# Kernel optimization log

Measured on AMD Instinct MI355X. Metric: run time of the kernel, lower is better.

The kernel has to match this reference:

```python
import jax, jax.numpy as jnp
import numpy as np

N_NODES = 100000
N_EDGES = 1600000
F_IN = 128
HID = 128
N_CLS = 40


def setup_inputs() -> dict:
    key = jax.random.key(0)
    ks = jax.random.split(key, 11)
    s = 0.05
    return {
        "X": jax.random.normal(ks[0], (N_NODES, F_IN), dtype=jnp.float32),
        "edge_index": jax.random.randint(ks[1], (2, N_EDGES), 0, N_NODES, dtype=jnp.int64),
        "enc_W": jax.random.normal(ks[2], (HID, F_IN), dtype=jnp.float32) * s,
        "enc_b": jax.random.normal(ks[3], (HID,), dtype=jnp.float32) * s,
        "W1": jax.random.normal(ks[4], (HID, HID), dtype=jnp.float32) * s,
        "b1": jax.random.normal(ks[5], (HID,), dtype=jnp.float32) * s,
        "W2": jax.random.normal(ks[6], (HID, HID), dtype=jnp.float32) * s,
        "b2": jax.random.normal(ks[7], (HID,), dtype=jnp.float32) * s,
        "dec_W": jax.random.normal(ks[8], (N_CLS, HID), dtype=jnp.float32) * s,
        "dec_b": jax.random.normal(ks[9], (N_CLS,), dtype=jnp.float32) * s,
    }


def reference(X, edge_index, enc_W, enc_b, W1, b1, W2, b2, dec_W, dec_b):
    N = X.shape[0]
    # --- add self-loops (PyG GCNConv default) ---
    loop = jnp.arange(N, dtype=edge_index.dtype)
    src = jnp.concatenate([edge_index[0], loop])  # message sources
    dst = jnp.concatenate([edge_index[1], loop])  # aggregation targets
    # --- symmetric normalization: D^{-1/2} A_hat D^{-1/2} ---
    deg = jax.ops.segment_sum(jnp.ones_like(src, dtype=X.dtype), dst, num_segments=N)
    dinv = jnp.where(deg > 0, jax.lax.rsqrt(deg), 0.0)
    norm = dinv[src] * dinv[dst]  # [E+N]

    def gcn_conv(x, W, b):
        h = x @ W.T                               # [N,H] linear transform
        msg = h[src] * norm[:, None]              # gather + scale  [E+N,H]
        agg = jax.ops.segment_sum(msg, dst, num_segments=N)  # scatter-sum
        return agg + b

    x = X @ enc_W.T + enc_b                       # encoder (single Linear)
    x = jax.nn.relu(gcn_conv(x, W1, b1))
    x = jax.nn.relu(gcn_conv(x, W2, b2))
    logits = x @ dec_W.T + dec_b                  # decoder (single Linear)
    return jax.nn.log_softmax(logits, axis=1)
```

## Files before the change

### kernel.cpp

```cpp
#include <hip/hip_runtime.h>
#include <hip/hip_bf16.h>
#include <cstdint>

typedef __bf16 bf16x8 __attribute__((ext_vector_type(8)));
typedef float  f32x4  __attribute__((ext_vector_type(4)));


__global__ __launch_bounds__(256) void bucket_hist_kernel(const int* __restrict__ dst,
                                                          int* __restrict__ bhist,
                                                          int E, int NBK, int shift) {
    __shared__ int lh[1024];
    int t = threadIdx.x;
    for (int i = t; i < 1024; i += 256) lh[i] = 0;
    __syncthreads();
#pragma unroll
    for (int v = 0; v < 4; ++v) {
        int idx = blockIdx.x * 4096 + (v * 256 + t) * 4;
        if (idx + 3 < E) {
            int4 d = *reinterpret_cast<const int4*>(&dst[idx]);
            atomicAdd(&lh[d.x >> shift], 1);
            atomicAdd(&lh[d.y >> shift], 1);
            atomicAdd(&lh[d.z >> shift], 1);
            atomicAdd(&lh[d.w >> shift], 1);
        } else {
            for (int k = 0; k < 4; ++k)
                if (idx + k < E) atomicAdd(&lh[dst[idx + k] >> shift], 1);
        }
    }
    __syncthreads();
    for (int i = t; i < NBK; i += 256)
        if (lh[i]) atomicAdd(&bhist[i], lh[i]);
}

__global__ __launch_bounds__(256) void bucket_scan_kernel(const int* __restrict__ bhist,
                                                          int* __restrict__ bbase,
                                                          int* __restrict__ bcur,
                                                          int NBK, int* __restrict__ offsetsN, int E) {
    int t = threadIdx.x;
    int v0[4]; int s = 0;
#pragma unroll
    for (int k = 0; k < 4; ++k) { int i = t * 4 + k; v0[k] = (i < NBK) ? bhist[i] : 0; s += v0[k]; }
    int lane = t & 63, w = t >> 6;
    int v = s;
#pragma unroll
    for (int o = 1; o < 64; o <<= 1) { int u = __shfl_up(v, o); if (lane >= o) v += u; }
    __shared__ int ws[4];
    if (lane == 63) ws[w] = v;
    __syncthreads();
    if (t == 0) { int r = 0; for (int i = 0; i < 4; ++i) { int x = ws[i]; ws[i] = r; r += x; } }
    __syncthreads();
    int run = ws[w] + (v - s);
#pragma unroll
    for (int k = 0; k < 4; ++k) {
        int i = t * 4 + k;
        if (i < NBK) { bbase[i] = run; bcur[i] = run; run += v0[k]; }
    }
    if (t == 255) bbase[NBK] = E;
    if (t == 0)   *offsetsN = E;
}

__global__ __launch_bounds__(256) void bin_edges_kernel(const int* __restrict__ src,
                                                        const int* __restrict__ dst,
                                                        int* __restrict__ bcur,
                                                        uint2* __restrict__ binned,
                                                        int E, int NBK, int shift) {
    __shared__ int lh[1024];
    int t = threadIdx.x;
    for (int i = t; i < 1024; i += 256) lh[i] = 0;
    __syncthreads();
    int sv[32], dv[32], rk[32];
#pragma unroll
    for (int v = 0; v < 8; ++v) {
        int idx = blockIdx.x * 8192 + (v * 256 + t) * 4;
        if (idx + 3 < E) {
            int4 s4 = *reinterpret_cast<const int4*>(&src[idx]);
            int4 d4 = *reinterpret_cast<const int4*>(&dst[idx]);
            sv[v * 4 + 0] = s4.x; sv[v * 4 + 1] = s4.y; sv[v * 4 + 2] = s4.z; sv[v * 4 + 3] = s4.w;
            dv[v * 4 + 0] = d4.x; dv[v * 4 + 1] = d4.y; dv[v * 4 + 2] = d4.z; dv[v * 4 + 3] = d4.w;
        } else {
            for (int k = 0; k < 4; ++k) {
                sv[v * 4 + k] = (idx + k < E) ? src[idx + k] : 0;
                dv[v * 4 + k] = (idx + k < E) ? dst[idx + k] : -1;
            }
        }
    }
#pragma unroll
    for (int k = 0; k < 32; ++k)
        if (dv[k] >= 0) rk[k] = atomicAdd(&lh[dv[k] >> shift], 1);
    __syncthreads();
    for (int i = t; i < NBK; i += 256) {
        int c = lh[i];
        lh[i] = c ? atomicAdd(&bcur[i], c) : 0;
    }
    __syncthreads();
#pragma unroll
    for (int k = 0; k < 32; ++k) {
        if (dv[k] >= 0) {
            int b = dv[k] >> shift;
            binned[lh[b] + rk[k]] = make_uint2((unsigned)sv[k], (unsigned)dv[k]);
        }
    }
}

__global__ __launch_bounds__(256) void bucket_build_kernel(const uint2* __restrict__ binned,
                                                           const int* __restrict__ bbase,
                                                           int* __restrict__ csr_src,
                                                           int* __restrict__ offsets,
                                                           float* __restrict__ dinv,
                                                           int N, int shift) {
    int b = blockIdx.x;
    int t = threadIdx.x;
    int node0 = b << shift;
    int npb = min(1 << shift, N - node0);
    int bb = bbase[b], be = bbase[b + 1];
    __shared__ int ncnt[256], npre[256], ncur[256];
    ncnt[t] = 0;
    __syncthreads();
    for (int e = bb + t; e < be; e += 256) {
        uint2 p = binned[e];
        atomicAdd(&ncnt[p.y - node0], 1);
    }
    __syncthreads();
    int deg = (t < npb) ? ncnt[t] : 0;
    int v = deg;
    int lane = t & 63, w = t >> 6;
#pragma unroll
    for (int o = 1; o < 64; o <<= 1) { int u = __shfl_up(v, o); if (lane >= o) v += u; }
    __shared__ int ws[4];
    if (lane == 63) ws[w] = v;
    __syncthreads();
    if (t == 0) { int r = 0; for (int i = 0; i < 4; ++i) { int x = ws[i]; ws[i] = r; r += x; } }
    __syncthreads();
    int pre = bb + ws[w] + v - deg;
    npre[t] = pre; ncur[t] = 0;
    __syncthreads();
    for (int e = bb + t; e < be; e += 256) {
        uint2 p = binned[e];
        int l = p.y - node0;
        int r = atomicAdd(&ncur[l], 1);
        csr_src[npre[l] + r] = (int)p.x;
    }
    if (t < npb) {
        int node = node0 + t;
        offsets[node] = pre;
        dinv[node] = rsqrtf((float)(deg + 1));
    }
}

__global__ __launch_bounds__(128) void prep_weights_kernel(const float* __restrict__ W1,
                                                           const float* __restrict__ encW,
                                                           const float* __restrict__ encb,
                                                           const float* __restrict__ W2,
                                                           const float* __restrict__ decW,
                                                           __hip_bfloat16* __restrict__ Wfb,
                                                           float* __restrict__ bff,
                                                           __hip_bfloat16* __restrict__ W2b,
                                                           __hip_bfloat16* __restrict__ decWb) {
    int i = blockIdx.x;
    int j = threadIdx.x;
    const float* w1r = W1 + (size_t)i * 128;
    float s0 = 0.f, s1 = 0.f, s2 = 0.f, s3 = 0.f;
    for (int k = 0; k < 128; k += 4) {
        s0 += w1r[k + 0] * encW[(size_t)(k + 0) * 128 + j];
        s1 += w1r[k + 1] * encW[(size_t)(k + 1) * 128 + j];
        s2 += w1r[k + 2] * encW[(size_t)(k + 2) * 128 + j];
        s3 += w1r[k + 3] * encW[(size_t)(k + 3) * 128 + j];
    }
    Wfb[(size_t)i * 128 + j] = __float2bfloat16((s0 + s1) + (s2 + s3));
    W2b[(size_t)i * 128 + j] = __float2bfloat16(W2[(size_t)i * 128 + j]);
    if (i < 48) decWb[(size_t)i * 128 + j] = __float2bfloat16(i < 40 ? decW[(size_t)i * 128 + j] : 0.f);
    float t = w1r[j] * encb[j];
#pragma unroll
    for (int o = 32; o; o >>= 1) t += __shfl_down(t, o);
    __shared__ float red[2];
    if ((j & 63) == 0) red[j >> 6] = t;
    __syncthreads();
    if (j == 0) bff[i] = red[0] + red[1];
}

__device__ inline bf16x8 cvt8(float4 lo, float4 hi) {
    union { unsigned short u[8]; bf16x8 v; } t;
    t.u[0] = __builtin_bit_cast(unsigned short, __float2bfloat16(lo.x));
    t.u[1] = __builtin_bit_cast(unsigned short, __float2bfloat16(lo.y));
    t.u[2] = __builtin_bit_cast(unsigned short, __float2bfloat16(lo.z));
    t.u[3] = __builtin_bit_cast(unsigned short, __float2bfloat16(lo.w));
    t.u[4] = __builtin_bit_cast(unsigned short, __float2bfloat16(hi.x));
    t.u[5] = __builtin_bit_cast(unsigned short, __float2bfloat16(hi.y));
    t.u[6] = __builtin_bit_cast(unsigned short, __float2bfloat16(hi.z));
    t.u[7] = __builtin_bit_cast(unsigned short, __float2bfloat16(hi.w));
    return t.v;
}

__global__ __launch_bounds__(256) void gemm_enc_kernel(const float* __restrict__ Ain,
                                                       const __hip_bfloat16* __restrict__ W,
                                                       const float* __restrict__ bias,
                                                       const float* __restrict__ dscale,
                                                       __hip_bfloat16* __restrict__ out, int M) {
    int lane = threadIdx.x & 63;
    int wave = threadIdx.x >> 6;
    int row0 = blockIdx.x * 128 + wave * 32;
    int kgrp = lane >> 4, cl = lane & 15;

    bf16x8 afrag[2][4];
#pragma unroll
    for (int rt = 0; rt < 2; ++rt) {
        int ar = row0 + rt * 16 + cl;
        if (ar >= M) ar = M - 1;
        const float* Ar = Ain + (size_t)ar * 128;
#pragma unroll
        for (int c = 0; c < 4; ++c) {
            const float4* q = reinterpret_cast<const float4*>(Ar + (4 * c + kgrp) * 8);
            afrag[rt][c] = cvt8(q[0], q[1]);
        }
    }

    f32x4 acc[2][8];
#pragma unroll
    for (int rt = 0; rt < 2; ++rt)
#pragma unroll
        for (int t = 0; t < 8; ++t) acc[rt][t] = {0.f, 0.f, 0.f, 0.f};

#pragma unroll
    for (int c = 0; c < 4; ++c) {
#pragma unroll
        for (int t = 0; t < 8; ++t) {
            bf16x8 bfrag = reinterpret_cast<const bf16x8*>(W + (size_t)(t * 16 + cl) * 128)[4 * c + kgrp];
            acc[0][t] = __builtin_amdgcn_mfma_f32_16x16x32_bf16(afrag[0][c], bfrag, acc[0][t], 0, 0, 0);
            acc[1][t] = __builtin_amdgcn_mfma_f32_16x16x32_bf16(afrag[1][c], bfrag, acc[1][t], 0, 0, 0);
        }
    }

#pragma unroll
    for (int rt = 0; rt < 2; ++rt) {
        int rbase = row0 + rt * 16 + kgrp * 4;
#pragma unroll
        for (int i = 0; i < 4; ++i) {
            int r = rbase + i;
            float sc = dscale[(r < M) ? r : (M - 1)];
#pragma unroll
            for (int t = 0; t < 8; ++t) {
                int col = t * 16 + cl;
                float v = (acc[rt][t][i] + bias[col]) * sc;
                unsigned int uv = __builtin_bit_cast(unsigned short, __float2bfloat16(v));
                unsigned int pv = (unsigned int)__shfl_xor((int)uv, 1);
                if (!(lane & 1) && r < M)
                    *reinterpret_cast<unsigned int*>(out + (size_t)r * 128 + col) = (uv & 0xffffu) | (pv << 16);
            }
        }
    }
}

template<int NPW>
__device__ __forceinline__ void agg_phase(const __hip_bfloat16* __restrict__ h,
                                          const int* __restrict__ csr_src,
                                          const int* __restrict__ offsets,
                                          const float* __restrict__ dinv,
                                          const float* __restrict__ bias,
                                          unsigned* lds, int tile0, int N) {
    int w = threadIdx.x >> 6, lane = threadIdx.x & 63;
    int bc = lane * 2;
    float2 bb = *reinterpret_cast<const float2*>(&bias[bc]);
    int base = tile0 + w * NPW;
    int oidx = base + (lane < NPW ? lane : NPW);
    if (oidx > N) oidx = N;
    int off = offsets[oidx];

    for (int i = 0; i < NPW; ++i) {
        int node = base + i;
        bool live = node < N;
        int nd = live ? node : N - 1;
        int j0 = __builtin_amdgcn_readfirstlane(__shfl(off, i));
        int j1 = __builtin_amdgcn_readfirstlane(__shfl(off, i + 1));

        float ax[8], ay[8];
        unsigned q0 = *reinterpret_cast<const unsigned*>(&h[(size_t)nd * 128 + bc]);
        ax[0] = __builtin_bit_cast(float, q0 << 16);
        ay[0] = __builtin_bit_cast(float, q0 & 0xffff0000u);
#pragma unroll
        for (int k = 1; k < 8; ++k) { ax[k] = 0.f; ay[k] = 0.f; }
        int j = j0;
        for (; j + 8 <= j1; j += 8) {
            int s[8];
#pragma unroll
            for (int k = 0; k < 8; ++k) s[k] = csr_src[j + k];
            unsigned q[8];
#pragma unroll
            for (int k = 0; k < 8; ++k)
                q[k] = *reinterpret_cast<const unsigned*>(&h[(size_t)s[k] * 128 + bc]);
#pragma unroll
            for (int k = 0; k < 8; ++k) {
                ax[k] += __builtin_bit_cast(float, q[k] << 16);
                ay[k] += __builtin_bit_cast(float, q[k] & 0xffff0000u);
            }
        }
        for (; j < j1; ++j) {
            int s0 = csr_src[j];
            unsigned q1 = *reinterpret_cast<const unsigned*>(&h[(size_t)s0 * 128 + bc]);
            ax[0] += __builtin_bit_cast(float, q1 << 16);
            ay[0] += __builtin_bit_cast(float, q1 & 0xffff0000u);
        }
        float sx = ((ax[0] + ax[1]) + (ax[2] + ax[3])) + ((ax[4] + ax[5]) + (ax[6] + ax[7]));
        float sy = ((ay[0] + ay[1]) + (ay[2] + ay[3])) + ((ay[4] + ay[5]) + (ay[6] + ay[7]));
        float dd = dinv[nd];
        float ox = fmaxf(dd * sx + bb.x, 0.f);
        float oy = fmaxf(dd * sy + bb.y, 0.f);
        unsigned ow = (unsigned)__builtin_bit_cast(unsigned short, __float2bfloat16(ox)) |
                      ((unsigned)__builtin_bit_cast(unsigned short, __float2bfloat16(oy)) << 16);
        if (!live) ow = 0u;
        int row = w * NPW + i;
        lds[row * 64 + (lane ^ ((row & 15) << 2))] = ow;
    }
}

__global__ __launch_bounds__(512) void agg_gemm_kernel(const __hip_bfloat16* __restrict__ h,
                                                       const int* __restrict__ csr_src,
                                                       const int* __restrict__ offsets,
                                                       const float* __restrict__ dinv,
                                                       const float* __restrict__ bias,
                                                       const __hip_bfloat16* __restrict__ W,
                                                       __hip_bfloat16* __restrict__ out, int N) {
    __shared__ unsigned lds[32 * 64];
    int tile0 = blockIdx.x * 32;
    agg_phase<4>(h, csr_src, offsets, dinv, bias, lds, tile0, N);
    __syncthreads();

    int lane = threadIdx.x & 63, w = threadIdx.x >> 6;
    int kgrp = lane >> 4, cl = lane & 15;
    int rt = w & 1, cq = w >> 1;
    bf16x8 afrag[4];
#pragma unroll
    for (int c = 0; c < 4; ++c) {
        int kk = 4 * c + kgrp;
        int row = rt * 16 + cl;
        afrag[c] = *reinterpret_cast<const bf16x8*>(&lds[row * 64 + ((kk * 4) ^ (cl << 2))]);
    }
    f32x4 acc[2];
#pragma unroll
    for (int t = 0; t < 2; ++t) acc[t] = {0.f, 0.f, 0.f, 0.f};
#pragma unroll
    for (int c = 0; c < 4; ++c)
#pragma unroll
        for (int t = 0; t < 2; ++t) {
            bf16x8 bfrag = reinterpret_cast<const bf16x8*>(W + (size_t)(cq * 32 + t * 16 + cl) * 128)[4 * c + kgrp];
            acc[t] = __builtin_amdgcn_mfma_f32_16x16x32_bf16(afrag[c], bfrag, acc[t], 0, 0, 0);
        }
#pragma unroll
    for (int i = 0; i < 4; ++i) {
        int r = tile0 + rt * 16 + kgrp * 4 + i;
        float sc = dinv[(r < N) ? r : (N - 1)];
#pragma unroll
        for (int t = 0; t < 2; ++t) {
            int col = cq * 32 + t * 16 + cl;
            float v = acc[t][i] * sc;
            unsigned uv = __builtin_bit_cast(unsigned short, __float2bfloat16(v));
            unsigned pv = (unsigned)__shfl_xor((int)uv, 1);
            if (!(lane & 1) && r < N)
                *reinterpret_cast<unsigned*>(out + (size_t)r * 128 + col) = (uv & 0xffffu) | (pv << 16);
        }
    }
}

__global__ __launch_bounds__(512) void agg_dec_kernel(const __hip_bfloat16* __restrict__ h,
                                                      const int* __restrict__ csr_src,
                                                      const int* __restrict__ offsets,
                                                      const float* __restrict__ dinv,
                                                      const float* __restrict__ bias,
                                                      const __hip_bfloat16* __restrict__ Wd,
                                                      const float* __restrict__ bd,
                                                      float* __restrict__ out, int N) {
    __shared__ unsigned lds[32 * 64];
    int tile0 = blockIdx.x * 32;
    agg_phase<4>(h, csr_src, offsets, dinv, bias, lds, tile0, N);
    __syncthreads();

    int lane = threadIdx.x & 63, w = threadIdx.x >> 6;
    if (w >= 2) return;
    int kgrp = lane >> 4, cl = lane & 15;
    bf16x8 afrag[4];
#pragma unroll
    for (int c = 0; c < 4; ++c) {
        int kk = 4 * c + kgrp;
        int row = w * 16 + cl;
        afrag[c] = *reinterpret_cast<const bf16x8*>(&lds[row * 64 + ((kk * 4) ^ (cl << 2))]);
    }
    f32x4 acc[3];
#pragma unroll
    for (int t = 0; t < 3; ++t) acc[t] = {0.f, 0.f, 0.f, 0.f};
#pragma unroll
    for (int c = 0; c < 4; ++c)
#pragma unroll
        for (int t = 0; t < 3; ++t) {
            bf16x8 bfrag = reinterpret_cast<const bf16x8*>(Wd + (size_t)(t * 16 + cl) * 128)[4 * c + kgrp];
            acc[t] = __builtin_amdgcn_mfma_f32_16x16x32_bf16(afrag[c], bfrag, acc[t], 0, 0, 0);
        }

    float v[3][4];
#pragma unroll
    for (int t = 0; t < 3; ++t) {
        int col = t * 16 + cl;
        float bv = (col < 40) ? bd[col] : 0.f;
#pragma unroll
        for (int i = 0; i < 4; ++i)
            v[t][i] = (col < 40) ? (acc[t][i] + bv) : -INFINITY;
    }
#pragma unroll
    for (int i = 0; i < 4; ++i) {
        float m = fmaxf(fmaxf(v[0][i], v[1][i]), v[2][i]);
#pragma unroll
        for (int o = 1; o < 16; o <<= 1) m = fmaxf(m, __shfl_xor(m, o));
        float s = 0.f;
#pragma unroll
        for (int t = 0; t < 3; ++t) s += (v[t][i] > -INFINITY) ? __expf(v[t][i] - m) : 0.f;
#pragma unroll
        for (int o = 1; o < 16; o <<= 1) s += __shfl_xor(s, o);
        float lse = __logf(s);
        int r = tile0 + w * 16 + kgrp * 4 + i;
        if (r < N) {
#pragma unroll
            for (int t = 0; t < 3; ++t) {
                int col = t * 16 + cl;
                if (col < 40) out[(size_t)r * 40 + col] = v[t][i] - m - lse;
            }
        }
    }
}

extern "C" void kernel_launch(void* const* d_in, const int* in_sizes, int n_in,
                              void* d_out, int out_size, void* d_ws, size_t ws_size,
                              hipStream_t stream) {
    const float* X    = (const float*)d_in[0];
    const int*   ei   = (const int*)d_in[1];
    const float* encW = (const float*)d_in[2];
    const float* encb = (const float*)d_in[3];
    const float* W1   = (const float*)d_in[4];
    const float* b1   = (const float*)d_in[5];
    const float* W2   = (const float*)d_in[6];
    const float* b2   = (const float*)d_in[7];
    const float* decW = (const float*)d_in[8];
    const float* decb = (const float*)d_in[9];

    const int N = in_sizes[0] / 128;
    const int E = in_sizes[1] / 2;
    const int* src = ei;
    const int* dst = ei + E;

    int shift = 7;
    while ((((N - 1) >> shift) + 1) > 1024) ++shift;
    const int NBK = ((N - 1) >> shift) + 1;

    uint8_t* p = (uint8_t*)d_ws;
    auto carve = [&](size_t bytes) -> void* {
        uint8_t* r = p;
        p += (bytes + 255) & ~(size_t)255;
        return (void*)r;
    };
    int*   offsets = (int*)carve((size_t)(N + 1) * 4);
    float* dinv    = (float*)carve((size_t)N * 4);
    int*   bhist   = (int*)carve(1025 * 4);
    int*   bbase   = (int*)carve(1025 * 4);
    int*   bcur    = (int*)carve(1024 * 4);
    int*   csr_src = (int*)carve((size_t)E * 4);
    __hip_bfloat16* Wfb   = (__hip_bfloat16*)carve(16384 * 2);
    __hip_bfloat16* W2b   = (__hip_bfloat16*)carve(16384 * 2);
    __hip_bfloat16* decWb = (__hip_bfloat16*)carve(48 * 128 * 2);
    float*          bff   = (float*)carve(128 * 4);
    __hip_bfloat16* xb    = (__hip_bfloat16*)carve((size_t)N * 128 * 2);
    __hip_bfloat16* hb    = (__hip_bfloat16*)carve((size_t)N * 128 * 2);
    uint2* binned = (uint2*)xb;

    prep_weights_kernel<<<128, 128, 0, stream>>>(W1, encW, encb, W2, decW, Wfb, bff, W2b, decWb);

    hipMemsetAsync(bhist, 0, (size_t)NBK * 4, stream);
    bucket_hist_kernel<<<(E + 4095) / 4096, 256, 0, stream>>>(dst, bhist, E, NBK, shift);
    bucket_scan_kernel<<<1, 256, 0, stream>>>(bhist, bbase, bcur, NBK, &offsets[N], E);
    bin_edges_kernel<<<(E + 8191) / 8192, 256, 0, stream>>>(src, dst, bcur, binned, E, NBK, shift);
    bucket_build_kernel<<<NBK, 256, 0, stream>>>(binned, bbase, csr_src, offsets, dinv, N, shift);

    int gblocks = (N + 127) / 128;
    int tblocks = (N + 31) / 32;
    gemm_enc_kernel<<<gblocks, 256, 0, stream>>>(X, Wfb, bff, dinv, hb, N);
    agg_gemm_kernel<<<tblocks, 512, 0, stream>>>(hb, csr_src, offsets, dinv, b1, W2b, xb, N);
    agg_dec_kernel<<<tblocks, 512, 0, stream>>>(xb, csr_src, offsets, dinv, b2, decWb, decb,
                                                (float*)d_out, N);
}
```

Baseline: 254.2 us.

## Sort nodes by degree for aggregation and pack binned edges into one word

Result: slower. 531.7 us (+109.2%).

```diff
diff --git a/kernel.cpp b/kernel.cpp
--- a/kernel.cpp
+++ b/kernel.cpp
@@ -62,10 +62,11 @@
 __global__ __launch_bounds__(256) void bin_edges_kernel(const int* __restrict__ src,
                                                         const int* __restrict__ dst,
                                                         int* __restrict__ bcur,
-                                                        uint2* __restrict__ binned,
+                                                        unsigned* __restrict__ binned,
                                                         int E, int NBK, int shift) {
     __shared__ int lh[1024];
     int t = threadIdx.x;
+    int mask = (1 << shift) - 1;
     for (int i = t; i < 1024; i += 256) lh[i] = 0;
     __syncthreads();
     int sv[32], dv[32], rk[32];
@@ -97,12 +98,12 @@
     for (int k = 0; k < 32; ++k) {
         if (dv[k] >= 0) {
             int b = dv[k] >> shift;
-            binned[lh[b] + rk[k]] = make_uint2((unsigned)sv[k], (unsigned)dv[k]);
-        }
-    }
-}
-
-__global__ __launch_bounds__(256) void bucket_build_kernel(const uint2* __restrict__ binned,
+            binned[lh[b] + rk[k]] = ((unsigned)sv[k] << shift) | (unsigned)(dv[k] & mask);
+        }
+    }
+}
+
+__global__ __launch_bounds__(256) void bucket_build_kernel(const unsigned* __restrict__ binned,
                                                            const int* __restrict__ bbase,
                                                            int* __restrict__ csr_src,
                                                            int* __restrict__ offsets,
@@ -113,12 +114,13 @@
     int node0 = b << shift;
     int npb = min(1 << shift, N - node0);
     int bb = bbase[b], be = bbase[b + 1];
+    int mask = (1 << shift) - 1;
     __shared__ int ncnt[256], npre[256], ncur[256];
     ncnt[t] = 0;
     __syncthreads();
     for (int e = bb + t; e < be; e += 256) {
-        uint2 p = binned[e];
-        atomicAdd(&ncnt[p.y - node0], 1);
+        unsigned p = binned[e];
+        atomicAdd(&ncnt[p & mask], 1);
     }
     __syncthreads();
     int deg = (t < npb) ? ncnt[t] : 0;
@@ -135,16 +137,64 @@
     npre[t] = pre; ncur[t] = 0;
     __syncthreads();
     for (int e = bb + t; e < be; e += 256) {
-        uint2 p = binned[e];
-        int l = p.y - node0;
+        unsigned p = binned[e];
+        int l = p & mask;
         int r = atomicAdd(&ncur[l], 1);
-        csr_src[npre[l] + r] = (int)p.x;
+        csr_src[npre[l] + r] = (int)(p >> shift);
     }
     if (t < npb) {
         int node = node0 + t;
         offsets[node] = pre;
         dinv[node] = rsqrtf((float)(deg + 1));
     }
+}
+
+__global__ __launch_bounds__(256) void deg_hist_kernel(const int* __restrict__ offsets,
+                                                       int* __restrict__ dh, int N) {
+    __shared__ int lh[512];
+    int t = threadIdx.x;
+    lh[t] = 0; lh[t + 256] = 0;
+    __syncthreads();
+    int i = blockIdx.x * 256 + t;
+    if (i < N) {
+        int deg = offsets[i + 1] - offsets[i];
+        atomicAdd(&lh[min(deg, 511)], 1);
+    }
+    __syncthreads();
+    if (lh[t]) atomicAdd(&dh[t], lh[t]);
+    if (lh[t + 256]) atomicAdd(&dh[t + 256], lh[t + 256]);
+}
+
+__global__ __launch_bounds__(256) void deg_scan_kernel(const int* __restrict__ dh,
+                                                       int* __restrict__ dcur) {
+    int t = threadIdx.x;
+    int v0 = dh[2 * t], v1 = dh[2 * t + 1];
+    int s = v0 + v1;
+    int lane = t & 63, w = t >> 6;
+    int v = s;
+#pragma unroll
+    for (int o = 1; o < 64; o <<= 1) { int u = __shfl_up(v, o); if (lane >= o) v += u; }
+    __shared__ int ws[4];
+    if (lane == 63) ws[w] = v;
+    __syncthreads();
+    if (t == 0) { int r = 0; for (int i = 0; i < 4; ++i) { int x = ws[i]; ws[i] = r; r += x; } }
+    __syncthreads();
+    int run = ws[w] + (v - s);
+    dcur[2 * t] = run;
+    dcur[2 * t + 1] = run + v0;
+}
+
+__global__ __launch_bounds__(256) void deg_scatter_kernel(const int* __restrict__ offsets,
+                                                          int* __restrict__ dcur,
+                                                          int* __restrict__ dorder,
+                                                          int2* __restrict__ off_deg, int N) {
+    int i = blockIdx.x * 256 + threadIdx.x;
+    if (i >= N) return;
+    int o0 = offsets[i];
+    int deg = offsets[i + 1] - o0;
+    int pos = atomicAdd(&dcur[min(deg, 511)], 1);
+    dorder[pos] = i;
+    off_deg[pos] = make_int2(o0, deg);
 }
 
 __global__ __launch_bounds__(128) void prep_weights_kernel(const float* __restrict__ W1,
@@ -253,27 +303,33 @@
 template<int NPW>
 __device__ __forceinline__ void agg_phase(const __hip_bfloat16* __restrict__ h,
                                           const int* __restrict__ csr_src,
-                                          const int* __restrict__ offsets,
+                                          const int* __restrict__ dorder,
+                                          const int2* __restrict__ off_deg,
                                           const float* __restrict__ dinv,
                                           const float* __restrict__ bias,
-                                          unsigned* lds, int tile0, int N) {
+                                          unsigned* lds, int* ndid, int tile0, int N) {
     int w = threadIdx.x >> 6, lane = threadIdx.x & 63;
     int bc = lane * 2;
     float2 bb = *reinterpret_cast<const float2*>(&bias[bc]);
     int base = tile0 + w * NPW;
-    int oidx = base + (lane < NPW ? lane : NPW);
-    if (oidx > N) oidx = N;
-    int off = offsets[oidx];
+
+    int2 od = make_int2(0, 0);
+    int nid = -1;
+    if (lane < NPW && base + lane < N) {
+        od  = off_deg[base + lane];
+        nid = dorder[base + lane];
+    }
 
     for (int i = 0; i < NPW; ++i) {
-        int node = base + i;
-        bool live = node < N;
-        int nd = live ? node : N - 1;
-        int j0 = __builtin_amdgcn_readfirstlane(__shfl(off, i));
-        int j1 = __builtin_amdgcn_readfirstlane(__shfl(off, i + 1));
+        int nd = __builtin_amdgcn_readfirstlane(__shfl(nid, i));
+        int j0 = __builtin_amdgcn_readfirstlane(__shfl(od.x, i));
+        int dg = __builtin_amdgcn_readfirstlane(__shfl(od.y, i));
+        bool live = nd >= 0;
+        int nds = live ? nd : 0;
+        int j1 = j0 + dg;
 
         float ax[8], ay[8];
-        unsigned q0 = *reinterpret_cast<const unsigned*>(&h[(size_t)nd * 128 + bc]);
+        unsigned q0 = *reinterpret_cast<const unsigned*>(&h[(size_t)nds * 128 + bc]);
         ax[0] = __builtin_bit_cast(float, q0 << 16);
         ay[0] = __builtin_bit_cast(float, q0 & 0xffff0000u);
 #pragma unroll
@@ -301,7 +357,7 @@
         }
         float sx = ((ax[0] + ax[1]) + (ax[2] + ax[3])) + ((ax[4] + ax[5]) + (ax[6] + ax[7]));
         float sy = ((ay[0] + ay[1]) + (ay[2] + ay[3])) + ((ay[4] + ay[5]) + (ay[6] + ay[7]));
-        float dd = dinv[nd];
+        float dd = dinv[nds];
         float ox = fmaxf(dd * sx + bb.x, 0.f);
         float oy = fmaxf(dd * sy + bb.y, 0.f);
         unsigned ow = (unsigned)__builtin_bit_cast(unsigned short, __float2bfloat16(ox)) |
@@ -309,19 +365,22 @@
         if (!live) ow = 0u;
         int row = w * NPW + i;
         lds[row * 64 + (lane ^ ((row & 15) << 2))] = ow;
+        if (lane == 0) ndid[row] = nd;
     }
 }
 
 __global__ __launch_bounds__(512) void agg_gemm_kernel(const __hip_bfloat16* __restrict__ h,
                                                        const int* __restrict__ csr_src,
-                                                       const int* __restrict__ offsets,
+                                                       const int* __restrict__ dorder,
+                                                       const int2* __restrict__ off_deg,
                                                        const float* __restrict__ dinv,
                                                        const float* __restrict__ bias,
                                                        const __hip_bfloat16* __restrict__ W,
                                                        __hip_bfloat16* __restrict__ out, int N) {
     __shared__ unsigned lds[32 * 64];
+    __shared__ int ndid[32];
     int tile0 = blockIdx.x * 32;
-    agg_phase<4>(h, csr_src, offsets, dinv, bias, lds, tile0, N);
+    agg_phase<4>(h, csr_src, dorder, off_deg, dinv, bias, lds, ndid, tile0, N);
     __syncthreads();
 
     int lane = threadIdx.x & 63, w = threadIdx.x >> 6;
@@ -346,31 +405,34 @@
         }
 #pragma unroll
     for (int i = 0; i < 4; ++i) {
-        int r = tile0 + rt * 16 + kgrp * 4 + i;
-        float sc = dinv[(r < N) ? r : (N - 1)];
+        int row = rt * 16 + kgrp * 4 + i;
+        int node = ndid[row];
+        float sc = dinv[(node >= 0) ? node : 0];
 #pragma unroll
         for (int t = 0; t < 2; ++t) {
             int col = cq * 32 + t * 16 + cl;
             float v = acc[t][i] * sc;
             unsigned uv = __builtin_bit_cast(unsigned short, __float2bfloat16(v));
             unsigned pv = (unsigned)__shfl_xor((int)uv, 1);
-            if (!(lane & 1) && r < N)
-                *reinterpret_cast<unsigned*>(out + (size_t)r * 128 + col) = (uv & 0xffffu) | (pv << 16);
+            if (!(lane & 1) && node >= 0)
+                *reinterpret_cast<unsigned*>(out + (size_t)node * 128 + col) = (uv & 0xffffu) | (pv << 16);
         }
     }
 }
 
 __global__ __launch_bounds__(512) void agg_dec_kernel(const __hip_bfloat16* __restrict__ h,
                                                       const int* __restrict__ csr_src,
-                                                      const int* __restrict__ offsets,
+                                                      const int* __restrict__ dorder,
+                                                      const int2* __restrict__ off_deg,
                                                       const float* __restrict__ dinv,
                                                       const float* __restrict__ bias,
                                                       const __hip_bfloat16* __restrict__ Wd,
                                                       const float* __restrict__ bd,
                                                       float* __restrict__ out, int N) {
     __shared__ unsigned lds[32 * 64];
+    __shared__ int ndid[32];
     int tile0 = blockIdx.x * 32;
-    agg_phase<4>(h, csr_src, offsets, dinv, bias, lds, tile0, N);
+    agg_phase<4>(h, csr_src, dorder, off_deg, dinv, bias, lds, ndid, tile0, N);
     __syncthreads();
 
     int lane = threadIdx.x & 63, w = threadIdx.x >> 6;
@@ -414,12 +476,13 @@
 #pragma unroll
         for (int o = 1; o < 16; o <<= 1) s += __shfl_xor(s, o);
         float lse = __logf(s);
-        int r = tile0 + w * 16 + kgrp * 4 + i;
-        if (r < N) {
+        int row = w * 16 + kgrp * 4 + i;
+        int node = ndid[row];
+        if (node >= 0) {
 #pragma unroll
             for (int t = 0; t < 3; ++t) {
                 int col = t * 16 + cl;
-                if (col < 40) out[(size_t)r * 40 + col] = v[t][i] - m - lse;
+                if (col < 40) out[(size_t)node * 40 + col] = v[t][i] - m - lse;
             }
         }
     }
@@ -459,6 +522,10 @@
     int*   bhist   = (int*)carve(1025 * 4);
     int*   bbase   = (int*)carve(1025 * 4);
     int*   bcur    = (int*)carve(1024 * 4);
+    int*   dh      = (int*)carve(512 * 4);
+    int*   dcur    = (int*)carve(512 * 4);
+    int*   dorder  = (int*)carve((size_t)N * 4);
+    int2*  off_deg = (int2*)carve((size_t)N * 8);
     int*   csr_src = (int*)carve((size_t)E * 4);
     __hip_bfloat16* Wfb   = (__hip_bfloat16*)carve(16384 * 2);
     __hip_bfloat16* W2b   = (__hip_bfloat16*)carve(16384 * 2);
@@ -466,7 +533,7 @@
     float*          bff   = (float*)carve(128 * 4);
     __hip_bfloat16* xb    = (__hip_bfloat16*)carve((size_t)N * 128 * 2);
     __hip_bfloat16* hb    = (__hip_bfloat16*)carve((size_t)N * 128 * 2);
-    uint2* binned = (uint2*)xb;
+    unsigned* binned = (unsigned*)xb;
 
     prep_weights_kernel<<<128, 128, 0, stream>>>(W1, encW, encb, W2, decW, Wfb, bff, W2b, decWb);
 
@@ -476,10 +543,15 @@
     bin_edges_kernel<<<(E + 8191) / 8192, 256, 0, stream>>>(src, dst, bcur, binned, E, NBK, shift);
     bucket_build_kernel<<<NBK, 256, 0, stream>>>(binned, bbase, csr_src, offsets, dinv, N, shift);
 
+    hipMemsetAsync(dh, 0, 512 * 4, stream);
+    deg_hist_kernel<<<(N + 255) / 256, 256, 0, stream>>>(offsets, dh, N);
+    deg_scan_kernel<<<1, 256, 0, stream>>>(dh, dcur);
+    deg_scatter_kernel<<<(N + 255) / 256, 256, 0, stream>>>(offsets, dcur, dorder, off_deg, N);
+
     int gblocks = (N + 127) / 128;
     int tblocks = (N + 31) / 32;
     gemm_enc_kernel<<<gblocks, 256, 0, stream>>>(X, Wfb, bff, dinv, hb, N);
-    agg_gemm_kernel<<<tblocks, 512, 0, stream>>>(hb, csr_src, offsets, dinv, b1, W2b, xb, N);
-    agg_dec_kernel<<<tblocks, 512, 0, stream>>>(xb, csr_src, offsets, dinv, b2, decWb, decb,
+    agg_gemm_kernel<<<tblocks, 512, 0, stream>>>(hb, csr_src, dorder, off_deg, dinv, b1, W2b, xb, N);
+    agg_dec_kernel<<<tblocks, 512, 0, stream>>>(xb, csr_src, dorder, off_deg, dinv, b2, decWb, decb,
                                                 (float*)d_out, N);
 }
```

## Pack binned edges to 32-bit and software-pipeline neighbor gathers across nodes

Applied to the files above, without the earlier changes.

After: 231.6 us. 8.9% less time.

```diff
diff --git a/kernel.cpp b/kernel.cpp
--- a/kernel.cpp
+++ b/kernel.cpp
@@ -62,10 +62,11 @@
 __global__ __launch_bounds__(256) void bin_edges_kernel(const int* __restrict__ src,
                                                         const int* __restrict__ dst,
                                                         int* __restrict__ bcur,
-                                                        uint2* __restrict__ binned,
+                                                        unsigned* __restrict__ binned,
                                                         int E, int NBK, int shift) {
     __shared__ int lh[1024];
     int t = threadIdx.x;
+    int mask = (1 << shift) - 1;
     for (int i = t; i < 1024; i += 256) lh[i] = 0;
     __syncthreads();
     int sv[32], dv[32], rk[32];
@@ -97,12 +98,12 @@
     for (int k = 0; k < 32; ++k) {
         if (dv[k] >= 0) {
             int b = dv[k] >> shift;
-            binned[lh[b] + rk[k]] = make_uint2((unsigned)sv[k], (unsigned)dv[k]);
-        }
-    }
-}
-
-__global__ __launch_bounds__(256) void bucket_build_kernel(const uint2* __restrict__ binned,
+            binned[lh[b] + rk[k]] = ((unsigned)sv[k] << shift) | (unsigned)(dv[k] & mask);
+        }
+    }
+}
+
+__global__ __launch_bounds__(256) void bucket_build_kernel(const unsigned* __restrict__ binned,
                                                            const int* __restrict__ bbase,
                                                            int* __restrict__ csr_src,
                                                            int* __restrict__ offsets,
@@ -113,12 +114,13 @@
     int node0 = b << shift;
     int npb = min(1 << shift, N - node0);
     int bb = bbase[b], be = bbase[b + 1];
+    int mask = (1 << shift) - 1;
     __shared__ int ncnt[256], npre[256], ncur[256];
     ncnt[t] = 0;
     __syncthreads();
     for (int e = bb + t; e < be; e += 256) {
-        uint2 p = binned[e];
-        atomicAdd(&ncnt[p.y - node0], 1);
+        unsigned p = binned[e];
+        atomicAdd(&ncnt[p & mask], 1);
     }
     __syncthreads();
     int deg = (t < npb) ? ncnt[t] : 0;
@@ -135,10 +137,10 @@
     npre[t] = pre; ncur[t] = 0;
     __syncthreads();
     for (int e = bb + t; e < be; e += 256) {
-        uint2 p = binned[e];
-        int l = p.y - node0;
+        unsigned p = binned[e];
+        int l = p & mask;
         int r = atomicAdd(&ncur[l], 1);
-        csr_src[npre[l] + r] = (int)p.x;
+        csr_src[npre[l] + r] = (int)(p >> shift);
     }
     if (t < npb) {
         int node = node0 + t;
@@ -252,7 +254,7 @@
 
 template<int NPW>
 __device__ __forceinline__ void agg_phase(const __hip_bfloat16* __restrict__ h,
-                                          const int* __restrict__ csr_src,
+                                          const int* __restrict__ csr,
                                           const int* __restrict__ offsets,
                                           const float* __restrict__ dinv,
                                           const float* __restrict__ bias,
@@ -265,43 +267,77 @@
     if (oidx > N) oidx = N;
     int off = offsets[oidx];
 
+    int j0a[NPW], dga[NPW], nda[NPW];
+    unsigned qs[NPW];
+#pragma unroll
     for (int i = 0; i < NPW; ++i) {
         int node = base + i;
+        nda[i] = __builtin_amdgcn_readfirstlane((node < N) ? node : (N - 1));
+        j0a[i] = __builtin_amdgcn_readfirstlane(__shfl(off, i));
+        int j1 = __builtin_amdgcn_readfirstlane(__shfl(off, i + 1));
+        dga[i] = j1 - j0a[i];
+        qs[i] = *reinterpret_cast<const unsigned*>(&h[(size_t)nda[i] * 128 + bc]);
+    }
+    int sc[NPW][8];
+#pragma unroll
+    for (int i = 0; i < NPW; ++i)
+#pragma unroll
+        for (int k = 0; k < 8; ++k)
+            sc[i][k] = csr[j0a[i] + k];
+    unsigned qn[8];
+#pragma unroll
+    for (int k = 0; k < 8; ++k)
+        qn[k] = *reinterpret_cast<const unsigned*>(&h[(size_t)sc[0][k] * 128 + bc]);
+
+#pragma unroll
+    for (int i = 0; i < NPW; ++i) {
+        int j0 = j0a[i], dg = dga[i];
+        int node = base + i;
         bool live = node < N;
-        int nd = live ? node : N - 1;
-        int j0 = __builtin_amdgcn_readfirstlane(__shfl(off, i));
-        int j1 = __builtin_amdgcn_readfirstlane(__shfl(off, i + 1));
+
+        unsigned qc[8];
+#pragma unroll
+        for (int k = 0; k < 8; ++k) qc[k] = qn[k];
+        if (i + 1 < NPW) {
+#pragma unroll
+            for (int k = 0; k < 8; ++k)
+                qn[k] = *reinterpret_cast<const unsigned*>(&h[(size_t)sc[i + 1][k] * 128 + bc]);
+        }
 
         float ax[8], ay[8];
-        unsigned q0 = *reinterpret_cast<const unsigned*>(&h[(size_t)nd * 128 + bc]);
-        ax[0] = __builtin_bit_cast(float, q0 << 16);
-        ay[0] = __builtin_bit_cast(float, q0 & 0xffff0000u);
+        ax[0] = __builtin_bit_cast(float, qs[i] << 16);
+        ay[0] = __builtin_bit_cast(float, qs[i] & 0xffff0000u);
 #pragma unroll
         for (int k = 1; k < 8; ++k) { ax[k] = 0.f; ay[k] = 0.f; }
-        int j = j0;
-        for (; j + 8 <= j1; j += 8) {
+
+#pragma unroll
+        for (int k = 0; k < 8; ++k) {
+            unsigned q = (k < dg) ? qc[k] : 0u;
+            ax[k] += __builtin_bit_cast(float, q << 16);
+            ay[k] += __builtin_bit_cast(float, q & 0xffff0000u);
+        }
+        int nb = (dg + 7) >> 3;
+        for (int b = 1; b < nb; ++b) {
+            int jb = j0 + 8 * b;
             int s[8];
 #pragma unroll
-            for (int k = 0; k < 8; ++k) s[k] = csr_src[j + k];
+            for (int k = 0; k < 8; ++k) s[k] = csr[jb + k];
             unsigned q[8];
 #pragma unroll
             for (int k = 0; k < 8; ++k)
                 q[k] = *reinterpret_cast<const unsigned*>(&h[(size_t)s[k] * 128 + bc]);
+            int rem = dg - 8 * b;
 #pragma unroll
             for (int k = 0; k < 8; ++k) {
-                ax[k] += __builtin_bit_cast(float, q[k] << 16);
-                ay[k] += __builtin_bit_cast(float, q[k] & 0xffff0000u);
+                unsigned qq = (k < rem) ? q[k] : 0u;
+                ax[k] += __builtin_bit_cast(float, qq << 16);
+                ay[k] += __builtin_bit_cast(float, qq & 0xffff0000u);
             }
         }
-        for (; j < j1; ++j) {
-            int s0 = csr_src[j];
-            unsigned q1 = *reinterpret_cast<const unsigned*>(&h[(size_t)s0 * 128 + bc]);
-            ax[0] += __builtin_bit_cast(float, q1 << 16);
-            ay[0] += __builtin_bit_cast(float, q1 & 0xffff0000u);
-        }
+
         float sx = ((ax[0] + ax[1]) + (ax[2] + ax[3])) + ((ax[4] + ax[5]) + (ax[6] + ax[7]));
         float sy = ((ay[0] + ay[1]) + (ay[2] + ay[3])) + ((ay[4] + ay[5]) + (ay[6] + ay[7]));
-        float dd = dinv[nd];
+        float dd = dinv[nda[i]];
         float ox = fmaxf(dd * sx + bb.x, 0.f);
         float oy = fmaxf(dd * sy + bb.y, 0.f);
         unsigned ow = (unsigned)__builtin_bit_cast(unsigned short, __float2bfloat16(ox)) |
@@ -312,16 +348,16 @@
     }
 }
 
-__global__ __launch_bounds__(512) void agg_gemm_kernel(const __hip_bfloat16* __restrict__ h,
-                                                       const int* __restrict__ csr_src,
-                                                       const int* __restrict__ offsets,
-                                                       const float* __restrict__ dinv,
-                                                       const float* __restrict__ bias,
-                                                       const __hip_bfloat16* __restrict__ W,
-                                                       __hip_bfloat16* __restrict__ out, int N) {
+__global__ __launch_bounds__(512, 8) void agg_gemm_kernel(const __hip_bfloat16* __restrict__ h,
+                                                          const int* __restrict__ csr,
+                                                          const int* __restrict__ offsets,
+                                                          const float* __restrict__ dinv,
+                                                          const float* __restrict__ bias,
+                                                          const __hip_bfloat16* __restrict__ W,
+                                                          __hip_bfloat16* __restrict__ out, int N) {
     __shared__ unsigned lds[32 * 64];
     int tile0 = blockIdx.x * 32;
-    agg_phase<4>(h, csr_src, offsets, dinv, bias, lds, tile0, N);
+    agg_phase<4>(h, csr, offsets, dinv, bias, lds, tile0, N);
     __syncthreads();
 
     int lane = threadIdx.x & 63, w = threadIdx.x >> 6;
@@ -360,17 +396,17 @@
     }
 }
 
-__global__ __launch_bounds__(512) void agg_dec_kernel(const __hip_bfloat16* __restrict__ h,
-                                                      const int* __restrict__ csr_src,
-                                                      const int* __restrict__ offsets,
-                                                      const float* __restrict__ dinv,
-                                                      const float* __restrict__ bias,
-                                                      const __hip_bfloat16* __restrict__ Wd,
-                                                      const float* __restrict__ bd,
-                                                      float* __restrict__ out, int N) {
+__global__ __launch_bounds__(512, 8) void agg_dec_kernel(const __hip_bfloat16* __restrict__ h,
+                                                         const int* __restrict__ csr,
+                                                         const int* __restrict__ offsets,
+                                                         const float* __restrict__ dinv,
+                                                         const float* __restrict__ bias,
+                                                         const __hip_bfloat16* __restrict__ Wd,
+                                                         const float* __restrict__ bd,
+                                                         float* __restrict__ out, int N) {
     __shared__ unsigned lds[32 * 64];
     int tile0 = blockIdx.x * 32;
-    agg_phase<4>(h, csr_src, offsets, dinv, bias, lds, tile0, N);
+    agg_phase<4>(h, csr, offsets, dinv, bias, lds, tile0, N);
     __syncthreads();
 
     int lane = threadIdx.x & 63, w = threadIdx.x >> 6;
@@ -459,18 +495,19 @@
     int*   bhist   = (int*)carve(1025 * 4);
     int*   bbase   = (int*)carve(1025 * 4);
     int*   bcur    = (int*)carve(1024 * 4);
-    int*   csr_src = (int*)carve((size_t)E * 4);
+    int*   csr_src = (int*)carve(((size_t)E + 8) * 4);
     __hip_bfloat16* Wfb   = (__hip_bfloat16*)carve(16384 * 2);
     __hip_bfloat16* W2b   = (__hip_bfloat16*)carve(16384 * 2);
     __hip_bfloat16* decWb = (__hip_bfloat16*)carve(48 * 128 * 2);
     float*          bff   = (float*)carve(128 * 4);
     __hip_bfloat16* xb    = (__hip_bfloat16*)carve((size_t)N * 128 * 2);
     __hip_bfloat16* hb    = (__hip_bfloat16*)carve((size_t)N * 128 * 2);
-    uint2* binned = (uint2*)xb;
+    unsigned* binned = (unsigned*)xb;
 
     prep_weights_kernel<<<128, 128, 0, stream>>>(W1, encW, encb, W2, decW, Wfb, bff, W2b, decWb);
 
     hipMemsetAsync(bhist, 0, (size_t)NBK * 4, stream);
+    hipMemsetAsync(csr_src + E, 0, 8 * 4, stream);
     bucket_hist_kernel<<<(E + 4095) / 4096, 256, 0, stream>>>(dst, bhist, E, NBK, shift);
     bucket_scan_kernel<<<1, 256, 0, stream>>>(bhist, bbase, bcur, NBK, &offsets[N], E);
     bin_edges_kernel<<<(E + 8191) / 8192, 256, 0, stream>>>(src, dst, bcur, binned, E, NBK, shift);
```
